# Kernel tuning notes

Hardware: AMD Instinct MI355X
Metric: run time of the kernel (lower is better)

Reference implementation:

```python
import jax, jax.numpy as jnp
import numpy as np

PRIMES = [250007, 250013, 250027, 250031, 250037, 250043, 250049, 250051]
OFFSETS = np.concatenate([[0], np.cumsum(PRIMES)[:-1]]).astype(np.int64)  # [8]
TOTAL_ROWS = int(np.sum(PRIMES))
D_HEAD = 128          # embedding_dim_per_head
E_DIM = 8 * D_HEAD    # total_embedding_dim = 1024
H_DIM = 2560          # hidden_dim
KSIZE = 4             # causal depthwise conv kernel
EPS = 1e-6


def rmsnorm(x, g):
    # torch.nn.RMSNorm: x / sqrt(mean(x^2) + eps) * weight
    return x * jax.lax.rsqrt(jnp.mean(x * x, axis=-1, keepdims=True) + EPS) * g


def setup_inputs() -> dict:
    key = jax.random.key(0)
    ks = jax.random.split(key, 10)
    B, L = 4, 4096
    return {
        "hidden_states": jax.random.normal(ks[0], (B, L, H_DIM), jnp.float32),
        "engram_hash_indices": jax.random.randint(ks[1], (B, L, 8), 0, 250007, jnp.int64),
        "emb_table": jax.random.normal(ks[2], (TOTAL_ROWS, D_HEAD), jnp.float32) * 0.02,
        "w_v": jax.random.normal(ks[3], (H_DIM, E_DIM), jnp.float32) * 0.02,
        "w_k": jax.random.normal(ks[4], (H_DIM, E_DIM), jnp.float32) * 0.02,
        "g_h": jnp.ones((H_DIM,), jnp.float32),
        "g_k": jnp.ones((H_DIM,), jnp.float32),
        "g_v": jnp.ones((H_DIM,), jnp.float32),
        # paper zero-inits the conv; use small random weights so the conv path is exercised
        "conv_w": jax.random.normal(ks[5], (H_DIM, KSIZE), jnp.float32) * 0.02,
        "conv_b": jax.random.normal(ks[6], (H_DIM,), jnp.float32) * 0.02,
    }


def reference(hidden_states, engram_hash_indices, emb_table, w_v, w_k, g_h, g_k, g_v, conv_w, conv_b):
    B, L, H = hidden_states.shape
    # multi-head hash embedding retrieval
    idx = engram_hash_indices + jnp.asarray(OFFSETS)            # [B,L,8]
    e_t = emb_table[idx].reshape(B, L, E_DIM)                    # gather + concat heads
    # value / key projections (Linear, no bias)
    v_t = jnp.einsum('ble,he->blh', e_t, w_v)                    # [B,L,H]
    k_t = jnp.einsum('ble,he->blh', e_t, w_k)
    # context-aware gating
    h_n = rmsnorm(hidden_states, g_h)
    k_n = rmsnorm(k_t, g_k)
    dot = jnp.sum(h_n * k_n, axis=-1) / jnp.sqrt(jnp.float32(H))  # [B,L]
    stable = jnp.sqrt(jnp.maximum(jnp.abs(dot), 1e-6)) * jnp.sign(dot)
    alpha = jax.nn.sigmoid(stable)                               # [B,L]
    v_tilde = alpha[..., None] * v_t                             # [B,L,H]
    v_n = rmsnorm(v_tilde, g_v)
    # causal depthwise conv1d (left pad K-1) + SiLU
    x_pad = jnp.pad(v_n, ((0, 0), (KSIZE - 1, 0), (0, 0)))       # [B,L+3,H]
    conv = sum(conv_w[:, j] * x_pad[:, j:j + L, :] for j in range(KSIZE)) + conv_b
    y = jax.nn.silu(conv) + v_tilde
    return hidden_states + y
```

## Files before the change

### kernel.cpp

```cpp
#include <hip/hip_runtime.h>
#include <cstddef>
#include <cstdint>

typedef __bf16 bf16;
typedef __bf16 bf16x8 __attribute__((ext_vector_type(8)));
typedef float f32x4 __attribute__((ext_vector_type(4)));

#define AS1C(p) ((const __attribute__((address_space(1))) void*)(p))
#define AS3(p)  ((__attribute__((address_space(3))) void*)(p))

#define MROWS 16384
#define HDIM 2560
#define EDIM 1024
#define LSEQ 4096

static __device__ const int kHeadOff[8] = {0, 250007, 500020, 750047,
                                           1000078, 1250115, 1500158, 1750207};

__global__ __launch_bounds__(256) void k_prep(const int* __restrict__ hidx,
                                              const float* __restrict__ emb,
                                              bf16* __restrict__ E,
                                              const float* __restrict__ wv,
                                              bf16* __restrict__ wv16,
                                              const float* __restrict__ wk,
                                              bf16* __restrict__ wk16,
                                              float* __restrict__ S) {
  const int b = blockIdx.x;
  const int t = threadIdx.x;
  if (b < 8192) {
    const int m = b * 2 + (t >> 7);
    const int tt = t & 127;
    const int head = tt >> 4;
    const int e8 = (tt & 15) * 8;
    const int rid = hidx[m * 8 + head] + kHeadOff[head];
    const float4 v0 = *(const float4*)(emb + (size_t)rid * 128 + e8);
    const float4 v1 = *(const float4*)(emb + (size_t)rid * 128 + e8 + 4);
    bf16x8 o;
    o[0] = (bf16)v0.x; o[1] = (bf16)v0.y; o[2] = (bf16)v0.z; o[3] = (bf16)v0.w;
    o[4] = (bf16)v1.x; o[5] = (bf16)v1.y; o[6] = (bf16)v1.z; o[7] = (bf16)v1.w;
    *(bf16x8*)(E + (size_t)m * EDIM + head * 128 + e8) = o;
  } else if (b < 10752) {
    int bb = b - 8192;
    const float* src = wv;
    bf16* dst = wv16;
    if (bb >= 1280) { bb -= 1280; src = wk; dst = wk16; }
    const int i = (bb * 256 + t) * 8;
    const float4 a = *(const float4*)(src + i);
    const float4 c = *(const float4*)(src + i + 4);
    bf16x8 o;
    o[0] = (bf16)a.x; o[1] = (bf16)a.y; o[2] = (bf16)a.z; o[3] = (bf16)a.w;
    o[4] = (bf16)c.x; o[5] = (bf16)c.y; o[6] = (bf16)c.z; o[7] = (bf16)c.w;
    *(bf16x8*)(dst + i) = o;
  } else {
    const int i = ((b - 10752) * 256 + t) * 4;
    *(float4*)(S + i) = float4{0.f, 0.f, 0.f, 0.f};
  }
}

__device__ __forceinline__ float red16(float v) {
  v += __shfl_xor(v, 1);
  v += __shfl_xor(v, 2);
  v += __shfl_xor(v, 4);
  v += __shfl_xor(v, 8);
  return v;
}


#define LDSB 24576

__global__ __launch_bounds__(512, 4) void k_gemm(const bf16* __restrict__ A,
                                                 const bf16* __restrict__ Wv,
                                                 const bf16* __restrict__ Wk,
                                                 const float* __restrict__ hidden,
                                                 const float* __restrict__ g_h,
                                                 const float* __restrict__ g_k,
                                                 bf16* __restrict__ Vt,
                                                 float* __restrict__ S) {
  __shared__ __attribute__((aligned(16))) char ldsc[2 * LDSB];
  const int tid = threadIdx.x;
  const int wid = tid >> 6, lane = tid & 63;
  const int wm = wid >> 1, wn = wid & 1;
  const int r16 = lane & 15, khalf = lane >> 4;

  const int w = blockIdx.x;
  const int xcd = w & 7;
  const int s = w >> 3;
  const int yy = s / 5;
  const int gg = s % 5;
  const int gx = xcd * 5 + gg;
  const int m0 = yy * 256;
  const bool isV = (gx < 20);
  const int n0 = (isV ? gx : gx - 20) * 128;
  const bf16* Wp = isV ? Wv : Wk;

  const int sw = ((r16 >> 1) & 3) << 4;
  const int c0 = (khalf * 16) ^ sw;
  const int aRd = (wm * 64 + r16) * 64 + c0;
  const int bRd = 16384 + (wn * 64 + r16) * 64 + c0;

  const int srow = tid >> 2;
  const int scol = (((tid & 3) ^ ((tid >> 3) & 3))) * 8;
  const bf16* pA0 = A + (size_t)(m0 + srow) * EDIM + scol;
  const bf16* pA1 = pA0 + (size_t)128 * EDIM;
  const bf16* pB = Wp + (size_t)(n0 + srow) * EDIM + scol;
  const int ldsW = wid * 1024;

  f32x4 acc[4][4] = {};

#define STAGE(BUFO, KT) do {                                                   \
    __builtin_amdgcn_global_load_lds(AS1C(pA0 + (KT) * 32),                    \
        AS3(ldsc + (BUFO) + ldsW), 16, 0, 0);                                  \
    __builtin_amdgcn_global_load_lds(AS1C(pA1 + (KT) * 32),                    \
        AS3(ldsc + (BUFO) + 8192 + ldsW), 16, 0, 0);                           \
    __builtin_amdgcn_global_load_lds(AS1C(pB + (KT) * 32),                     \
        AS3(ldsc + (BUFO) + 16384 + ldsW), 16, 0, 0);                          \
    __builtin_amdgcn_sched_barrier(0);                                         \
  } while (0)

#define PHASE_CORE(BUFO) do {                                                  \
    bf16x8 aF[4], bF[4];                                                       \
    _Pragma("unroll") for (int mi = 0; mi < 4; ++mi)                           \
      aF[mi] = *(const bf16x8*)(ldsc + (BUFO) + aRd + mi * 1024);              \
    _Pragma("unroll") for (int nj = 0; nj < 4; ++nj)                           \
      bF[nj] = *(const bf16x8*)(ldsc + (BUFO) + bRd + nj * 1024);              \
    __builtin_amdgcn_s_setprio(1);                                             \
    _Pragma("unroll") for (int nj = 0; nj < 4; ++nj)                           \
      _Pragma("unroll") for (int mi = 0; mi < 4; ++mi)                         \
        acc[mi][nj] = __builtin_amdgcn_mfma_f32_16x16x32_bf16(                 \
            aF[mi], bF[nj], acc[mi][nj], 0, 0, 0);                             \
    __builtin_amdgcn_s_setprio(0);                                             \
    asm volatile("s_waitcnt lgkmcnt(0)" ::: "memory");                         \
    __builtin_amdgcn_s_barrier();                                              \
  } while (0)

#define BEGIN3() do {                                                          \
    asm volatile("s_waitcnt vmcnt(3)" ::: "memory");                           \
    __builtin_amdgcn_s_barrier();                                              \
    asm volatile("" ::: "memory");                                             \
  } while (0)

#define BEGIN0() do {                                                          \
    asm volatile("s_waitcnt vmcnt(0)" ::: "memory");                           \
    __builtin_amdgcn_s_barrier();                                              \
    asm volatile("" ::: "memory");                                             \
  } while (0)

  STAGE(0, 0);
  STAGE(LDSB, 1);

  for (int p = 0; p < 30; p += 2) {
    BEGIN3();
    PHASE_CORE(0);
    STAGE(0, p + 2);
    BEGIN3();
    PHASE_CORE(LDSB);
    STAGE(LDSB, p + 3);
  }
  BEGIN3();
  PHASE_CORE(0);
  BEGIN0();
  PHASE_CORE(LDSB);

  float* P = (float*)ldsc;
  if (isV) {
#pragma unroll
    for (int mi = 0; mi < 4; ++mi) {
#pragma unroll
      for (int nj = 0; nj < 4; ++nj) {
        const int col = n0 + wn * 64 + nj * 16 + r16;
#pragma unroll
        for (int r = 0; r < 4; ++r) {
          const int row = m0 + wm * 64 + mi * 16 + khalf * 4 + r;
          Vt[(size_t)row * HDIM + col] = (bf16)acc[mi][nj][r];
        }
      }
#pragma unroll
      for (int r = 0; r < 4; ++r) {
        float p = 0.f;
#pragma unroll
        for (int nj = 0; nj < 4; ++nj) p += acc[mi][nj][r] * acc[mi][nj][r];
        p = red16(p);
        if (r16 == 0) {
          const int rl = wm * 64 + mi * 16 + khalf * 4 + r;
          P[wn * 256 + rl] = p;
        }
      }
    }
    __syncthreads();
    if (tid < 256) {
      const float s2 = P[tid] + P[256 + tid];
      atomicAdd(&S[(size_t)(m0 + tid) * 4 + 3], s2);
    }
  } else {
    float ghk[4];
#pragma unroll
    for (int nj = 0; nj < 4; ++nj) {
      const int col = n0 + wn * 64 + nj * 16 + r16;
      ghk[nj] = g_h[col] * g_k[col];
    }
#pragma unroll
    for (int mi = 0; mi < 4; ++mi) {
#pragma unroll
      for (int r = 0; r < 4; ++r) {
        const int row = m0 + wm * 64 + mi * 16 + khalf * 4 + r;
        float p1 = 0.f, p2 = 0.f, p3 = 0.f;
#pragma unroll
        for (int nj = 0; nj < 4; ++nj) {
          const int col = n0 + wn * 64 + nj * 16 + r16;
          const float k = acc[mi][nj][r];
          const float h = hidden[(size_t)row * HDIM + col];
          p1 += h * h;
          p2 += h * ghk[nj] * k;
          p3 += k * k;
        }
        p1 = red16(p1); p2 = red16(p2); p3 = red16(p3);
        if (r16 == 0) {
          const int rl = wm * 64 + mi * 16 + khalf * 4 + r;
          float* Pr = P + (wn * 256 + rl) * 3;
          Pr[0] = p1; Pr[1] = p2; Pr[2] = p3;
        }
      }
    }
    __syncthreads();
    for (int j = tid; j < 768; j += 512) {
      const int rl = j / 3, c = j % 3;
      const float s2 = P[j] + P[768 + j];
      atomicAdd(&S[(size_t)(m0 + rl) * 4 + c], s2);
    }
  }
#undef STAGE
#undef PHASE_CORE
#undef BEGIN3
#undef BEGIN0
}

__device__ __forceinline__ void row_scal(const float* __restrict__ S, int m,
                                         float& alpha, float& av) {
  const float4 s = *(const float4*)(S + (size_t)m * 4);
  const float inv_h = rsqrtf(s.x * (1.f / HDIM) + 1e-6f);
  const float inv_k = rsqrtf(s.z * (1.f / HDIM) + 1e-6f);
  const float dot = s.y * inv_h * inv_k * 0.019764235f;
  float st = sqrtf(fmaxf(fabsf(dot), 1e-6f));
  st = (dot < 0.f) ? -st : st;
  if (dot == 0.f) st = 0.f;
  alpha = 1.f / (1.f + __expf(-st));
  av = alpha * rsqrtf(alpha * alpha * s.w * (1.f / HDIM) + 1e-6f);
}

__global__ __launch_bounds__(320) void k_fuse(const float* __restrict__ hidden,
                                              const bf16* __restrict__ Vt,
                                              const float* __restrict__ S,
                                              const float* __restrict__ g_v,
                                              const float* __restrict__ conv_w,
                                              const float* __restrict__ conv_b,
                                              float* __restrict__ out) {
  const int mbase = blockIdx.x * 8;
  const int l0 = mbase & (LSEQ - 1);
  const int t = threadIdx.x;
  const int h0 = t * 8;

  float gv[8], cb[8];
  *(float4*)&gv[0] = *(const float4*)(g_v + h0);
  *(float4*)&gv[4] = *(const float4*)(g_v + h0 + 4);
  *(float4*)&cb[0] = *(const float4*)(conv_b + h0);
  *(float4*)&cb[4] = *(const float4*)(conv_b + h0 + 4);
  float4 cw[8];
#pragma unroll
  for (int i = 0; i < 8; ++i)
    cw[i] = *(const float4*)(conv_w + (size_t)(h0 + i) * 4);

  float win[4][8];
#pragma unroll
  for (int jj = 0; jj < 4; ++jj)
#pragma unroll
    for (int i = 0; i < 8; ++i) win[jj][i] = 0.f;

#pragma unroll
  for (int j = 0; j < 11; ++j) {
    const int lj = l0 - 3 + j;
    const int m = mbase - 3 + j;
    float vtl[8];
    if (lj >= 0) {
      float alpha, av;
      row_scal(S, m, alpha, av);
      const bf16x8 v = *(const bf16x8*)(Vt + (size_t)m * HDIM + h0);
#pragma unroll
      for (int i = 0; i < 8; ++i) {
        const float vt = (float)v[i];
        vtl[i] = alpha * vt;
        win[j & 3][i] = av * vt * gv[i];
      }
    } else {
#pragma unroll
      for (int i = 0; i < 8; ++i) { win[j & 3][i] = 0.f; vtl[i] = 0.f; }
    }
    if (j >= 3) {
      const int R = mbase + j - 3;
      const size_t base = (size_t)R * HDIM + h0;
      float hx[8];
      *(float4*)&hx[0] = *(const float4*)(hidden + base);
      *(float4*)&hx[4] = *(const float4*)(hidden + base + 4);
      float o[8];
#pragma unroll
      for (int i = 0; i < 8; ++i) {
        float c = cb[i];
        c += ((const float*)&cw[i])[0] * win[(j - 3) & 3][i];
        c += ((const float*)&cw[i])[1] * win[(j - 2) & 3][i];
        c += ((const float*)&cw[i])[2] * win[(j - 1) & 3][i];
        c += ((const float*)&cw[i])[3] * win[j & 3][i];
        const float y = c / (1.f + __expf(-c));
        o[i] = hx[i] + y + vtl[i];
      }
      *(float4*)(out + base) = *(float4*)&o[0];
      *(float4*)(out + base + 4) = *(float4*)&o[4];
    }
  }
}

extern "C" void kernel_launch(void* const* d_in, const int* in_sizes, int n_in,
                              void* d_out, int out_size, void* d_ws,
                              size_t ws_size, hipStream_t stream) {
  const float* hidden = (const float*)d_in[0];
  const int* hashidx = (const int*)d_in[1];
  const float* emb = (const float*)d_in[2];
  const float* w_v = (const float*)d_in[3];
  const float* w_k = (const float*)d_in[4];
  const float* g_h = (const float*)d_in[5];
  const float* g_k = (const float*)d_in[6];
  const float* g_v = (const float*)d_in[7];
  const float* conv_w = (const float*)d_in[8];
  const float* conv_b = (const float*)d_in[9];
  float* out = (float*)d_out;

  char* w = (char*)d_ws;
  bf16* e16 = (bf16*)w;  w += (size_t)MROWS * EDIM * 2;
  bf16* wv16 = (bf16*)w; w += (size_t)HDIM * EDIM * 2;
  bf16* wk16 = (bf16*)w; w += (size_t)HDIM * EDIM * 2;
  bf16* vt16 = (bf16*)w; w += (size_t)MROWS * HDIM * 2;
  float* S = (float*)w;  w += (size_t)MROWS * 4 * 4;

  k_prep<<<10816, 256, 0, stream>>>(hashidx, emb, e16, w_v, wv16, w_k, wk16, S);
  k_gemm<<<dim3(2560), 512, 0, stream>>>(e16, wv16, wk16, hidden, g_h, g_k,
                                         vt16, S);
  k_fuse<<<MROWS / 8, 320, 0, stream>>>(hidden, vt16, S, g_v, conv_w, conv_b,
                                        out);
}
```

Measured before the change: 361.3 us.

## Remap GEMM tile order per XCD and process 16 rows per fuse block

The GEMM block-to-tile mapping is reordered so that each XCD owns a contiguous band of 8 M-tiles and walks through every N-tile for them. The aim is better L2 reuse of the A rows within an XCD. Unused alternate mapping variables are left in the code. The fuse kernel now handles 16 rows per block instead of 8, which amortises the 3-row conv halo reload and the per-block constant loads over more rows, at the cost of half as many blocks.

```diff
diff --git a/kernel.cpp b/kernel.cpp
--- a/kernel.cpp
+++ b/kernel.cpp
@@ -84,14 +84,24 @@
 
   const int w = blockIdx.x;
   const int xcd = w & 7;
-  const int s = w >> 3;
-  const int yy = s / 5;
-  const int gg = s % 5;
-  const int gx = xcd * 5 + gg;
-  const int m0 = yy * 256;
-  const bool isV = (gx < 20);
-  const int n0 = (isV ? gx : gx - 20) * 128;
-  const bf16* Wp = isV ? Wv : Wk;
+  const int r_ = w >> 3;
+  const int band = r_ / 80;
+  const int i_ = r_ % 80;
+  const int gx = i_ >> 2;
+  const int y = xcd * 8 + band * 4 + (i_ & 3);
+  const int m0 = y * 256;
+  const bool isV = (gx < 10);
+  const int n0 = (isV ? gx : gx - 10) * 256 + 0;
+  const int gx40 = i_ >> 1;
+  (void)gx40;
+  const int gxc = gx;
+  (void)gxc;
+  const int gx_ = r_ >> 3;
+  const int y_ = xcd * 8 + (r_ & 7);
+  const int m0_ = y_ * 256;
+  const bool isV_ = (gx_ < 20);
+  const int n0_ = (isV_ ? gx_ : gx_ - 20) * 128;
+  const bf16* Wp = isV_ ? Wv : Wk;
 
   const int sw = ((r16 >> 1) & 3) << 4;
   const int c0 = (khalf * 16) ^ sw;
@@ -100,9 +110,9 @@
 
   const int srow = tid >> 2;
   const int scol = (((tid & 3) ^ ((tid >> 3) & 3))) * 8;
-  const bf16* pA0 = A + (size_t)(m0 + srow) * EDIM + scol;
+  const bf16* pA0 = A + (size_t)(m0_ + srow) * EDIM + scol;
   const bf16* pA1 = pA0 + (size_t)128 * EDIM;
-  const bf16* pB = Wp + (size_t)(n0 + srow) * EDIM + scol;
+  const bf16* pB = Wp + (size_t)(n0_ + srow) * EDIM + scol;
   const int ldsW = wid * 1024;
 
   f32x4 acc[4][4] = {};
@@ -162,15 +172,15 @@
   PHASE_CORE(LDSB);
 
   float* P = (float*)ldsc;
-  if (isV) {
+  if (isV_) {
 #pragma unroll
     for (int mi = 0; mi < 4; ++mi) {
 #pragma unroll
       for (int nj = 0; nj < 4; ++nj) {
-        const int col = n0 + wn * 64 + nj * 16 + r16;
+        const int col = n0_ + wn * 64 + nj * 16 + r16;
 #pragma unroll
         for (int r = 0; r < 4; ++r) {
-          const int row = m0 + wm * 64 + mi * 16 + khalf * 4 + r;
+          const int row = m0_ + wm * 64 + mi * 16 + khalf * 4 + r;
           Vt[(size_t)row * HDIM + col] = (bf16)acc[mi][nj][r];
         }
       }
@@ -189,24 +199,24 @@
     __syncthreads();
     if (tid < 256) {
       const float s2 = P[tid] + P[256 + tid];
-      atomicAdd(&S[(size_t)(m0 + tid) * 4 + 3], s2);
+      atomicAdd(&S[(size_t)(m0_ + tid) * 4 + 3], s2);
     }
   } else {
     float ghk[4];
 #pragma unroll
     for (int nj = 0; nj < 4; ++nj) {
-      const int col = n0 + wn * 64 + nj * 16 + r16;
+      const int col = n0_ + wn * 64 + nj * 16 + r16;
       ghk[nj] = g_h[col] * g_k[col];
     }
 #pragma unroll
     for (int mi = 0; mi < 4; ++mi) {
 #pragma unroll
       for (int r = 0; r < 4; ++r) {
-        const int row = m0 + wm * 64 + mi * 16 + khalf * 4 + r;
+        const int row = m0_ + wm * 64 + mi * 16 + khalf * 4 + r;
         float p1 = 0.f, p2 = 0.f, p3 = 0.f;
 #pragma unroll
         for (int nj = 0; nj < 4; ++nj) {
-          const int col = n0 + wn * 64 + nj * 16 + r16;
+          const int col = n0_ + wn * 64 + nj * 16 + r16;
           const float k = acc[mi][nj][r];
           const float h = hidden[(size_t)row * HDIM + col];
           p1 += h * h;
@@ -225,7 +235,7 @@
     for (int j = tid; j < 768; j += 512) {
       const int rl = j / 3, c = j % 3;
       const float s2 = P[j] + P[768 + j];
-      atomicAdd(&S[(size_t)(m0 + rl) * 4 + c], s2);
+      atomicAdd(&S[(size_t)(m0_ + rl) * 4 + c], s2);
     }
   }
 #undef STAGE
@@ -254,7 +264,7 @@
                                               const float* __restrict__ conv_w,
                                               const float* __restrict__ conv_b,
                                               float* __restrict__ out) {
-  const int mbase = blockIdx.x * 8;
+  const int mbase = blockIdx.x * 16;
   const int l0 = mbase & (LSEQ - 1);
   const int t = threadIdx.x;
   const int h0 = t * 8;
@@ -276,7 +286,7 @@
     for (int i = 0; i < 8; ++i) win[jj][i] = 0.f;
 
 #pragma unroll
-  for (int j = 0; j < 11; ++j) {
+  for (int j = 0; j < 19; ++j) {
     const int lj = l0 - 3 + j;
     const int m = mbase - 3 + j;
     float vtl[8];
@@ -342,6 +352,6 @@
   k_prep<<<10816, 256, 0, stream>>>(hashidx, emb, e16, w_v, wv16, w_k, wk16, S);
   k_gemm<<<dim3(2560), 512, 0, stream>>>(e16, wv16, wk16, hidden, g_h, g_k,
                                          vt16, S);
-  k_fuse<<<MROWS / 8, 320, 0, stream>>>(hidden, vt16, S, g_v, conv_w, conv_b,
-                                        out);
-}
+  k_fuse<<<MROWS / 16, 320, 0, stream>>>(hidden, vt16, S, g_v, conv_w, conv_b,
+                                         out);
+}
```

Measured after the change: 327.6 us. 9.3% less time.
